# Optimization experiments

Measured on AMD Instinct MI355X. Metric: run time of the kernel, lower is better.

## Reference

```python
import jax, jax.numpy as jnp
import numpy as np

V = 30000      # vocab_size
D = 300        # t_embed
H = 4          # GATv2 heads
C = 300        # per-head out channels (hidden_dim = t_embed)
HID = 768      # hidden_size
B = 2
T = 800
NEG = 0.2      # GATv2 negative_slope default


def gatv2_layer(x, src, dst, Wl, bl, Wr, br, att, bias):
    """PyG GATv2Conv, eval mode, add_self_loops=True, concat=True.
    x: [N, Fin]; src/dst: [E] (src->dst message flow).
    Wl/Wr: [Fin, H*C]; bl/br: [H*C]; att: [H, C]; bias: [H*C].
    """
    N = x.shape[0]
    xl = (x @ Wl + bl).reshape(N, H, C)   # source transform
    xr = (x @ Wr + br).reshape(N, H, C)   # target transform
    loops = jnp.arange(N)
    s = jnp.concatenate([src, loops])
    d = jnp.concatenate([dst, loops])
    e = jax.nn.leaky_relu(xl[s] + xr[d], NEG)          # [E', H, C]
    logits = jnp.einsum('ehc,hc->eh', e, att)           # [E', H]
    # scatter-softmax over incoming edges per target node
    mx = jax.ops.segment_max(logits, d, num_segments=N)  # [N, H]
    ex = jnp.exp(logits - mx[d])
    den = jax.ops.segment_sum(ex, d, num_segments=N)
    alpha = ex / den[d]                                   # [E', H]
    out = jax.ops.segment_sum(alpha[:, :, None] * xl[s], d, num_segments=N)
    return out.reshape(N, H * C) + bias


def setup_inputs() -> dict:
    key = jax.random.key(0)
    ks = jax.random.split(key, 20)
    sc = 0.05
    inp = {
        'kg_enc_input': jax.random.randint(ks[0], (B, T, 3), 0, V),
        'embeddings': jax.random.normal(ks[1], (V, D), jnp.float32),
        # conv1: GATv2Conv(D, C, heads=H)
        'Wl1': jax.random.normal(ks[2], (D, H * C), jnp.float32) * sc,
        'bl1': jnp.zeros((H * C,), jnp.float32),
        'Wr1': jax.random.normal(ks[3], (D, H * C), jnp.float32) * sc,
        'br1': jnp.zeros((H * C,), jnp.float32),
        'att1': jax.random.normal(ks[4], (H, C), jnp.float32) * sc,
        'bias1': jnp.zeros((H * C,), jnp.float32),
        # conv2: GATv2Conv(4*C, C, heads=H)
        'Wl2': jax.random.normal(ks[5], (H * C, H * C), jnp.float32) * sc,
        'bl2': jnp.zeros((H * C,), jnp.float32),
        'Wr2': jax.random.normal(ks[6], (H * C, H * C), jnp.float32) * sc,
        'br2': jnp.zeros((H * C,), jnp.float32),
        'att2': jax.random.normal(ks[7], (H, C), jnp.float32) * sc,
        'bias2': jnp.zeros((H * C,), jnp.float32),
        # post_mp: Linear(4*C, C) -> Dropout -> Linear(C, D)
        'Wp1': jax.random.normal(ks[8], (H * C, C), jnp.float32) * sc,
        'bp1': jnp.zeros((C,), jnp.float32),
        'Wp2': jax.random.normal(ks[9], (C, D), jnp.float32) * sc,
        'bp2': jnp.zeros((D,), jnp.float32),
        # lii: Linear(3*D, HID, bias=False)
        'Wlii': jax.random.normal(ks[10], (3 * D, HID), jnp.float32) * sc,
    }
    return inp


def reference(kg_enc_input, embeddings, Wl1, bl1, Wr1, br1, att1, bias1,
              Wl2, bl2, Wr2, br2, att2, bias2, Wp1, bp1, Wp2, bp2, Wlii):
    # original GAT.forward detaches x -> no grad to embedding table
    x0 = jax.lax.stop_gradient(embeddings)

    def per_sample(kg):  # kg: [T, 3]
        head, rel, tail = kg[:, 0], kg[:, 1], kg[:, 2]
        # edge_list = cat([[head;rel], [rel;tail]], dim=1)
        src = jnp.concatenate([head, rel])
        dst = jnp.concatenate([rel, tail])
        h = gatv2_layer(x0, src, dst, Wl1, bl1, Wr1, br1, att1, bias1)
        h = jax.nn.relu(h)                 # dropout: eval mode, identity
        h = gatv2_layer(h, src, dst, Wl2, bl2, Wr2, br2, att2, bias2)
        h = jax.nn.relu(h)
        w = (h @ Wp1 + bp1) @ Wp2 + bp2    # post_mp, [V, D]
        # per-triple gather + concat of (h, r, t) node embeddings
        return jnp.concatenate([w[head], w[rel], w[tail]], axis=-1)  # [T, 3D]

    final = jax.vmap(per_sample)(kg_enc_input)   # [B, T, 3D]
    return final @ Wlii                           # [B, T, HID]
```

## Files before the change

kernel.cpp:

```cpp
#include <hip/hip_runtime.h>
#include <hip/hip_bf16.h>

#define V 30000
#define D 300
#define H 4
#define C 300
#define HC 1200
#define B 2
#define T 800
#define E 1600
#define MAXM 2400
#define NEG 0.2f
#define SCAN_CH ((MAXM + 255) / 256)

#define MR 2432
#define KD 320
#define KHC 1216
#define NLR 2432
#define WB_LD 320
#define KF2 960

typedef __attribute__((ext_vector_type(8))) unsigned short u16x8;
typedef __attribute__((ext_vector_type(8))) short s16x8;
typedef __attribute__((ext_vector_type(4))) float f32x4;

__device__ inline unsigned short f2b(float v) {
    unsigned u = __float_as_uint(v);
    unsigned r = (u + 0x7FFFu + ((u >> 16) & 1u)) >> 16;
    return (unsigned short)r;
}
__device__ inline float b2f(unsigned short u) {
    return __uint_as_float(((unsigned)u) << 16);
}

#define GLOAD_LDS16(g, l) __builtin_amdgcn_global_load_lds( \
    (const __attribute__((address_space(1))) void*)(g), \
    (__attribute__((address_space(3))) void*)(l), 16, 0, 0)


__global__ void k_init(int* map, int* list, int* mcnt) {
    int i = blockIdx.x * blockDim.x + threadIdx.x;
    if (i < B * V) map[i] = -1;
    if (i < B * MAXM) list[i] = 0;
    if (i < B) mcnt[i] = 0;
}

__global__ void k_mark(const int* __restrict__ kg, int* map) {
    int i = blockIdx.x * blockDim.x + threadIdx.x;
    if (i >= B * T * 3) return;
    int b = i / (T * 3);
    map[b * V + kg[i]] = 1;
}

__global__ void k_compact(int* map, int* list, int* mcnt) {
    int b = blockIdx.y;
    int i = blockIdx.x * 256 + threadIdx.x;
    bool pred = (i < V) && (map[b * V + i] == 1);
    unsigned long long m = __ballot(pred);
    int lane = threadIdx.x & 63;
    int wid = threadIdx.x >> 6;
    __shared__ int wcnt[4];
    __shared__ int base;
    if (lane == 0) wcnt[wid] = __popcll(m);
    __syncthreads();
    if (threadIdx.x == 0) {
        int t = 0;
#pragma unroll
        for (int w2 = 0; w2 < 4; ++w2) { int c = wcnt[w2]; wcnt[w2] = t; t += c; }
        base = t ? atomicAdd(&mcnt[b], t) : 0;
    }
    __syncthreads();
    if (pred) {
        int idx = base + wcnt[wid] + __popcll(m & ((1ull << lane) - 1ull));
        map[b * V + i] = idx;
        list[b * MAXM + idx] = i;
    }
}

__global__ __launch_bounds__(256) void k_graph(const int* __restrict__ kg,
                                               const int* __restrict__ map,
                                               int* __restrict__ off_g,
                                               int* __restrict__ csr,
                                               int* __restrict__ tric) {
    int b = blockIdx.x;
    int tid = threadIdx.x;
    __shared__ int sdeg[MAXM];
    __shared__ int soff[MAXM + 1];
    __shared__ int ses[E];
    __shared__ int sed[E];
    __shared__ int ts[256];
    for (int j = tid; j < MAXM; j += 256) sdeg[j] = 0;
    __syncthreads();
    for (int t = tid; t < T; t += 256) {
        const int* kk = kg + ((long)b * T + t) * 3;
        int hc = map[b * V + kk[0]];
        int rc = map[b * V + kk[1]];
        int tc = map[b * V + kk[2]];
        ses[t] = hc;     sed[t] = rc;
        ses[T + t] = rc; sed[T + t] = tc;
        atomicAdd(&sdeg[rc], 1);
        atomicAdd(&sdeg[tc], 1);
        int* tr = tric + ((long)b * T + t) * 3;
        tr[0] = hc; tr[1] = rc; tr[2] = tc;
    }
    __syncthreads();
    int base = tid * SCAN_CH;
    int loc[SCAN_CH];
    int sum = 0;
#pragma unroll
    for (int j = 0; j < SCAN_CH; ++j) {
        int v = (base + j < MAXM) ? sdeg[base + j] : 0;
        sum += v; loc[j] = sum;
    }
    ts[tid] = sum; __syncthreads();
    for (int s = 1; s < 256; s <<= 1) {
        int v = (tid >= s) ? ts[tid - s] : 0;
        __syncthreads();
        ts[tid] += v;
        __syncthreads();
    }
    int excl = (tid > 0) ? ts[tid - 1] : 0;
#pragma unroll
    for (int j = 0; j < SCAN_CH; ++j)
        if (base + j < MAXM) soff[base + j + 1] = excl + loc[j];
    if (tid == 0) soff[0] = 0;
    __syncthreads();
    for (int j = tid; j < MAXM; j += 256) sdeg[j] = 0;
    __syncthreads();
    for (int e = tid; e < E; e += 256) {
        int d = sed[e];
        int pos = soff[d] + atomicAdd(&sdeg[d], 1);
        csr[b * E + pos] = ses[e];
    }
    for (int j = tid; j <= MAXM; j += 256) off_g[b * (MAXM + 1) + j] = soff[j];
}

__global__ void k_wt_all(const float* __restrict__ Wl1, const float* __restrict__ Wr1,
                         const float* __restrict__ Wl2, const float* __restrict__ Wr2,
                         const float* __restrict__ Wp1, const float* __restrict__ Wp2,
                         const float* __restrict__ Wlii,
                         const float* __restrict__ bl1, const float* __restrict__ br1,
                         const float* __restrict__ bl2, const float* __restrict__ br2,
                         const float* __restrict__ bp1, const float* __restrict__ bp2,
                         unsigned short* Wlr1t, unsigned short* Wlr2t,
                         unsigned short* Wp2t, unsigned short* Wp1b,
                         unsigned short* Wft2,
                         float* blr1, float* blr2, float* bp12) {
    const int KT[6]  = {10, 10, 38, 38, 10, 30};
    const int CUM[10] = {0, 380, 760, 2204, 3648, 3748, 4468, 4508, 4518, 4520};
    int bid = blockIdx.x;
    int task = 0;
    while (bid >= CUM[task + 1]) ++task;
    int local = bid - CUM[task];
    int tx = threadIdx.x, ty = threadIdx.y;
    int tid = ty * 32 + tx;

    if (task == 6) {
        int r0 = local * 32;
#pragma unroll
        for (int p = 0; p < 4; ++p) {
            int row = r0 + ty + p * 8;
#pragma unroll
            for (int j = 0; j < 10; ++j) {
                int c = tx + j * 32;
                unsigned short v = 0;
                if (row < 1200 && c < 300) v = f2b(Wp1[(long)row * 300 + c]);
                Wp1b[(long)row * 320 + c] = v;
            }
        }
        return;
    }
    if (task == 7) {
        int c = local * 256 + tid;
        if (c < NLR) {
            float v1 = 0.f, v2 = 0.f;
            if (c < 1200) { v1 = bl1[c]; v2 = bl2[c]; }
            else if (c >= 1216 && c < 2416) { v1 = br1[c - 1216]; v2 = br2[c - 1216]; }
            blr1[c] = v1; blr2[c] = v2;
        }
        return;
    }
    if (task == 8) {
        int n = local * 256 + tid;
        if (n < 300) {
            float s = bp2[n];
            for (int m = 0; m < 300; ++m) s += bp1[m] * Wp2[(long)m * 300 + n];
            bp12[n] = s;
        }
        return;
    }

    __shared__ float t[32][33];
    if (task == 5) {
        int kt = local % 30, nt = local / 30;
        int k0 = kt * 32, n0 = nt * 32;
#pragma unroll
        for (int p = 0; p < 4; ++p) {
            int gk = k0 + ty + p * 8, n = n0 + tx;
            int pp = (gk >= 640) ? 2 : (gk >= 320 ? 1 : 0);
            int kc = gk - pp * 320;
            t[ty + p * 8][tx] = (kc < 300) ? Wlii[(long)(300 * pp + kc) * 768 + n] : 0.f;
        }
        __syncthreads();
#pragma unroll
        for (int p = 0; p < 4; ++p) {
            int n = n0 + ty + p * 8, gk = k0 + tx;
            Wft2[(long)n * 960 + gk] = f2b(t[tx][ty + p * 8]);
        }
        return;
    }

    int kt = local % KT[task], nt = local / KT[task];
    const float* W; unsigned short* Wt; int K, N, Kp;
    switch (task) {
        case 0: W = Wl1;  Wt = Wlr1t;                     K = 300;  N = 1200; Kp = KD;  break;
        case 1: W = Wr1;  Wt = Wlr1t + (long)1216 * KD;   K = 300;  N = 1200; Kp = KD;  break;
        case 2: W = Wl2;  Wt = Wlr2t;                     K = 1200; N = 1200; Kp = KHC; break;
        case 3: W = Wr2;  Wt = Wlr2t + (long)1216 * KHC;  K = 1200; N = 1200; Kp = KHC; break;
        default: W = Wp2; Wt = Wp2t;                      K = 300;  N = 300;  Kp = KD;  break;
    }
    int k0 = kt * 32, n0 = nt * 32;
#pragma unroll
    for (int p = 0; p < 4; ++p) {
        int k = k0 + ty + p * 8, n = n0 + tx;
        t[ty + p * 8][tx] = (k < K && n < N) ? W[(long)k * N + n] : 0.f;
    }
    __syncthreads();
#pragma unroll
    for (int p = 0; p < 4; ++p) {
        int n = n0 + ty + p * 8, k = k0 + tx;
        Wt[(long)n * Kp + k] = f2b(t[tx][ty + p * 8]);
    }
}

__global__ void k_embgather(const float* __restrict__ emb, const int* __restrict__ list,
                            unsigned short* __restrict__ Eb) {
    int b = blockIdx.y, i = blockIdx.x;
    int src = list[b * MAXM + i];
    const float* e = emb + (long)src * D;
    unsigned short* o = Eb + ((long)b * MR + i) * KD;
    int c = threadIdx.x;
    if (c < 75) {
        float4 v = *(const float4*)(e + c * 4);
        ushort4 u;
        u.x = f2b(v.x); u.y = f2b(v.y); u.z = f2b(v.z); u.w = f2b(v.w);
        *(ushort4*)(o + c * 4) = u;
    } else if (c < 80) {
        *(ushort4*)(o + c * 4) = make_ushort4(0, 0, 0, 0);
    }
}

__device__ inline void tile_decode(int& m0, int& n0) {
    int nbx = gridDim.x, nby = gridDim.y;
    int nwg = nbx * nby;
    int wg = blockIdx.y * nbx + blockIdx.x;
    int q = nwg >> 3, r8 = nwg & 7;
    int xcd = wg & 7, idx = wg >> 3;
    int L = (xcd < r8 ? xcd * (q + 1) : r8 * (q + 1) + (xcd - r8) * q) + idx;
    const int G = 4;
    int band = L / (G * nbx);
    int first = band * G;
    int sz = min(G, nby - first);
    int rem = L - band * G * nbx;
    int by = first + rem % sz;
    int bx = rem / sz;
    m0 = by * 128; n0 = bx * 128;
}

__global__ __launch_bounds__(256) void k_mgemm(
    const unsigned short* __restrict__ A, long sA, int lda,
    const unsigned short* __restrict__ Wt, int ldw,
    const float* __restrict__ bias,
    int M, int N, int K,
    float* __restrict__ outF, long sF, int ldf,
    unsigned short* __restrict__ outB, long sB, int ldb_) {
    int b = blockIdx.z;
    A += (long)b * sA;
    __shared__ unsigned short As[2][128][32];
    __shared__ unsigned short Bs[2][128][32];
    int tid = threadIdx.x;
    int m0, n0; tile_decode(m0, n0);

    int w = tid >> 6, lane = tid & 63;
    int wr = (w >> 1) * 64, wc = (w & 1) * 64;
    int fr = lane & 15, fq = lane >> 4;
    int r0 = tid >> 2, sg = tid & 3;
    int swz = (sg ^ ((r0 >> 1) & 3)) * 8;
    const unsigned short* Ap  = A  + (long)(m0 + r0) * lda + swz;
    const unsigned short* Ap2 = A  + (long)(m0 + r0 + 64) * lda + swz;
    const unsigned short* Bp  = Wt + (long)(n0 + r0) * ldw + swz;
    const unsigned short* Bp2 = Wt + (long)(n0 + r0 + 64) * ldw + swz;

    f32x4 acc[4][4] = {};
    GLOAD_LDS16(Ap,  &As[0][r0][sg * 8]);
    GLOAD_LDS16(Ap2, &As[0][r0 + 64][sg * 8]);
    GLOAD_LDS16(Bp,  &Bs[0][r0][sg * 8]);
    GLOAD_LDS16(Bp2, &Bs[0][r0 + 64][sg * 8]);
    __syncthreads();
    int cur = 0;
    for (int k0 = 0; k0 < K; k0 += 32) {
        int nxt = cur ^ 1;
        if (k0 + 32 < K) {
            GLOAD_LDS16(Ap + k0 + 32,  &As[nxt][r0][sg * 8]);
            GLOAD_LDS16(Ap2 + k0 + 32, &As[nxt][r0 + 64][sg * 8]);
            GLOAD_LDS16(Bp + k0 + 32,  &Bs[nxt][r0][sg * 8]);
            GLOAD_LDS16(Bp2 + k0 + 32, &Bs[nxt][r0 + 64][sg * 8]);
        }
        s16x8 af[4], bfr[4];
#pragma unroll
        for (int m = 0; m < 4; ++m) {
            int rr = wr + m * 16 + fr;
            af[m] = *(const s16x8*)&As[cur][rr][(fq ^ ((rr >> 1) & 3)) * 8];
        }
#pragma unroll
        for (int n = 0; n < 4; ++n) {
            int rr = wc + n * 16 + fr;
            bfr[n] = *(const s16x8*)&Bs[cur][rr][(fq ^ ((rr >> 1) & 3)) * 8];
        }
#pragma unroll
        for (int m = 0; m < 4; ++m)
#pragma unroll
            for (int n = 0; n < 4; ++n)
                acc[m][n] = __builtin_amdgcn_mfma_f32_16x16x32_bf16(af[m], bfr[n], acc[m][n], 0, 0, 0);
        __syncthreads();
        cur = nxt;
    }
    float* oF = outF ? outF + (long)b * sF : nullptr;
    unsigned short* oB = outB ? outB + (long)b * sB : nullptr;
#pragma unroll
    for (int m = 0; m < 4; ++m) {
        int rb = m0 + wr + m * 16 + fq * 4;
#pragma unroll
        for (int n = 0; n < 4; ++n) {
            int col = n0 + wc + n * 16 + fr;
#pragma unroll
            for (int j = 0; j < 4; ++j) {
                int row = rb + j;
                if (row >= M) continue;
                if (col < N) {
                    float v = acc[m][n][j] + (bias ? bias[col] : 0.f);
                    if (oF) oF[(long)row * ldf + col] = v;
                    if (oB) oB[(long)row * ldb_ + col] = f2b(v);
                } else if (oB && col < ldb_) {
                    oB[(long)row * ldb_ + col] = 0;
                }
            }
        }
    }
}

__global__ __launch_bounds__(256) void k_fgemm(
    const unsigned short* __restrict__ wb, long sW,
    const int* __restrict__ tric,
    const unsigned short* __restrict__ Wft2,
    float* __restrict__ out) {
    int b = blockIdx.z;
    const unsigned short* wB = wb + (long)b * sW;
    const int* tr = tric + (long)b * T * 3;
    float* oF = out + (long)b * T * 768;
    __shared__ unsigned short As[2][128][32];
    __shared__ unsigned short Bs[2][128][32];
    int tid = threadIdx.x;
    int m0, n0; tile_decode(m0, n0);

    int w = tid >> 6, lane = tid & 63;
    int wr = (w >> 1) * 64, wc = (w & 1) * 64;
    int fr = lane & 15, fq = lane >> 4;
    int r0 = tid >> 2, sg = tid & 3;
    int swz = (sg ^ ((r0 >> 1) & 3)) * 8;

    int gm  = m0 + r0;
    int gm2 = gm + 64;
    int t1 = min(gm, T - 1) * 3, t2 = min(gm2, T - 1) * 3;
    int tr_a[3] = {tr[t1], tr[t1 + 1], tr[t1 + 2]};
    int tr_b[3] = {tr[t2], tr[t2 + 1], tr[t2 + 2]};

    const unsigned short* Bp  = Wft2 + (long)(n0 + r0) * KF2 + swz;
    const unsigned short* Bp2 = Wft2 + (long)(n0 + r0 + 64) * KF2 + swz;

    auto stage = [&](int buf, int k0) {
        int kk = k0 + swz;
        int p_ = (kk >= 640) ? 2 : (kk >= 320 ? 1 : 0);
        int kc = kk - p_ * 320;
        GLOAD_LDS16(wB + (long)tr_a[p_] * WB_LD + kc, &As[buf][r0][sg * 8]);
        GLOAD_LDS16(wB + (long)tr_b[p_] * WB_LD + kc, &As[buf][r0 + 64][sg * 8]);
        GLOAD_LDS16(Bp + k0,  &Bs[buf][r0][sg * 8]);
        GLOAD_LDS16(Bp2 + k0, &Bs[buf][r0 + 64][sg * 8]);
    };

    f32x4 acc[4][4] = {};
    stage(0, 0);
    __syncthreads();
    int cur = 0;
    for (int k0 = 0; k0 < KF2; k0 += 32) {
        int nxt = cur ^ 1;
        if (k0 + 32 < KF2) stage(nxt, k0 + 32);
        s16x8 af[4], bfr[4];
#pragma unroll
        for (int m = 0; m < 4; ++m) {
            int rr = wr + m * 16 + fr;
            af[m] = *(const s16x8*)&As[cur][rr][(fq ^ ((rr >> 1) & 3)) * 8];
        }
#pragma unroll
        for (int n = 0; n < 4; ++n) {
            int rr = wc + n * 16 + fr;
            bfr[n] = *(const s16x8*)&Bs[cur][rr][(fq ^ ((rr >> 1) & 3)) * 8];
        }
#pragma unroll
        for (int m = 0; m < 4; ++m)
#pragma unroll
            for (int n = 0; n < 4; ++n)
                acc[m][n] = __builtin_amdgcn_mfma_f32_16x16x32_bf16(af[m], bfr[n], acc[m][n], 0, 0, 0);
        __syncthreads();
        cur = nxt;
    }
#pragma unroll
    for (int m = 0; m < 4; ++m) {
        int rb = m0 + wr + m * 16 + fq * 4;
#pragma unroll
        for (int n = 0; n < 4; ++n) {
            int col = n0 + wc + n * 16 + fr;
#pragma unroll
            for (int j = 0; j < 4; ++j) {
                int row = rb + j;
                if (row < T) oF[(long)row * 768 + col] = acc[m][n][j];
            }
        }
    }
}

__global__ __launch_bounds__(256) void k_att(
    const unsigned short* __restrict__ XLR,
    const int* __restrict__ off, const int* __restrict__ csr,
    const float* __restrict__ att, const float* __restrict__ bias,
    unsigned short* __restrict__ OUT) {
    const long sX = (long)MR * NLR;
    const long sO = (long)MR * KHC;
    int b = blockIdx.y;
    int i = blockIdx.x;
    const unsigned short* xl = XLR + (long)b * sX;
    const unsigned short* xr = xl + 1216;
    unsigned short* out = OUT + (long)b * sO;
    int lane = threadIdx.x & 63;
    int h = threadIdx.x >> 6;
    int c0 = lane * 4;
    int c1 = 256 + c0;
    bool tail = lane < 11;

    float xrf[8], attf[8];
    {
        const unsigned short* xp = xr + (long)i * NLR + h * C;
        ushort4 u0 = *(const ushort4*)(xp + c0);
        ushort4 u1 = tail ? *(const ushort4*)(xp + c1) : make_ushort4(0, 0, 0, 0);
        xrf[0] = b2f(u0.x); xrf[1] = b2f(u0.y); xrf[2] = b2f(u0.z); xrf[3] = b2f(u0.w);
        xrf[4] = b2f(u1.x); xrf[5] = b2f(u1.y); xrf[6] = b2f(u1.z); xrf[7] = b2f(u1.w);
        float4 a0 = *(const float4*)(att + h * C + c0);
        attf[0] = a0.x; attf[1] = a0.y; attf[2] = a0.z; attf[3] = a0.w;
        if (tail) {
            float4 a1 = *(const float4*)(att + h * C + c1);
            attf[4] = a1.x; attf[5] = a1.y; attf[6] = a1.z; attf[7] = a1.w;
        } else { attf[4] = attf[5] = attf[6] = attf[7] = 0.f; }
    }
    int o0 = off[b * (MAXM + 1) + i];
    int dg = off[b * (MAXM + 1) + i + 1] - o0;
    const int* cs = csr + b * E;

    float mx = -3e38f, den = 0.f;
    float acc[8] = {0.f, 0.f, 0.f, 0.f, 0.f, 0.f, 0.f, 0.f};
    auto step = [&](int s) {
        const unsigned short* xp = xl + (long)s * NLR + h * C;
        ushort4 v0 = *(const ushort4*)(xp + c0);
        ushort4 v1 = tail ? *(const ushort4*)(xp + c1) : make_ushort4(0, 0, 0, 0);
        float xv[8];
        xv[0] = b2f(v0.x); xv[1] = b2f(v0.y); xv[2] = b2f(v0.z); xv[3] = b2f(v0.w);
        xv[4] = b2f(v1.x); xv[5] = b2f(v1.y); xv[6] = b2f(v1.z); xv[7] = b2f(v1.w);
        float part = 0.f;
#pragma unroll
        for (int j = 0; j < 8; ++j) {
            float v = xv[j] + xrf[j];
            v = v > 0.f ? v : NEG * v;
            part += attf[j] * v;
        }
#pragma unroll
        for (int m = 1; m < 64; m <<= 1) part += __shfl_xor(part, m);
        float mn = fmaxf(mx, part);
        float sc = __expf(mx - mn);
        float p = __expf(part - mn);
        den = den * sc + p;
#pragma unroll
        for (int j = 0; j < 8; ++j) acc[j] = acc[j] * sc + p * xv[j];
        mx = mn;
    };
    step(i);
    for (int e = 0; e < dg; ++e) step(cs[o0 + e]);

    float inv = 1.f / den;
    unsigned short* op = out + (long)i * KHC + h * C;
    {
        float4 b0 = *(const float4*)(bias + h * C + c0);
        ushort4 s0;
        float v;
        v = acc[0] * inv + b0.x; s0.x = f2b(v > 0.f ? v : 0.f);
        v = acc[1] * inv + b0.y; s0.y = f2b(v > 0.f ? v : 0.f);
        v = acc[2] * inv + b0.z; s0.z = f2b(v > 0.f ? v : 0.f);
        v = acc[3] * inv + b0.w; s0.w = f2b(v > 0.f ? v : 0.f);
        *(ushort4*)(op + c0) = s0;
        if (tail) {
            float4 b1 = *(const float4*)(bias + h * C + c1);
            ushort4 s1;
            v = acc[4] * inv + b1.x; s1.x = f2b(v > 0.f ? v : 0.f);
            v = acc[5] * inv + b1.y; s1.y = f2b(v > 0.f ? v : 0.f);
            v = acc[6] * inv + b1.z; s1.z = f2b(v > 0.f ? v : 0.f);
            v = acc[7] * inv + b1.w; s1.w = f2b(v > 0.f ? v : 0.f);
            *(ushort4*)(op + c1) = s1;
        }
    }
    if (h == 0 && lane < KHC - HC)
        out[(long)i * KHC + HC + lane] = 0;
}

extern "C" void kernel_launch(void* const* d_in, const int* in_sizes, int n_in,
                              void* d_out, int out_size, void* d_ws, size_t ws_size,
                              hipStream_t stream) {
    const int*   kg    = (const int*)d_in[0];
    const float* emb   = (const float*)d_in[1];
    const float* Wl1   = (const float*)d_in[2];
    const float* bl1   = (const float*)d_in[3];
    const float* Wr1   = (const float*)d_in[4];
    const float* br1   = (const float*)d_in[5];
    const float* att1  = (const float*)d_in[6];
    const float* bias1 = (const float*)d_in[7];
    const float* Wl2   = (const float*)d_in[8];
    const float* bl2   = (const float*)d_in[9];
    const float* Wr2   = (const float*)d_in[10];
    const float* br2   = (const float*)d_in[11];
    const float* att2  = (const float*)d_in[12];
    const float* bias2 = (const float*)d_in[13];
    const float* Wp1   = (const float*)d_in[14];
    const float* bp1   = (const float*)d_in[15];
    const float* Wp2   = (const float*)d_in[16];
    const float* bp2   = (const float*)d_in[17];
    const float* Wlii  = (const float*)d_in[18];
    float* out = (float*)d_out;

    char* ws = (char*)d_ws;
    size_t o = 0;
    auto alloc = [&](size_t bytes) -> void* {
        void* p = ws + o;
        o = (o + bytes + 255) & ~(size_t)255;
        return p;
    };
    int* map  = (int*)alloc(sizeof(int) * B * V);
    int* list = (int*)alloc(sizeof(int) * B * MAXM);
    int* mcnt = (int*)alloc(sizeof(int) * B);
    int* off  = (int*)alloc(sizeof(int) * B * (MAXM + 1));
    int* csr  = (int*)alloc(sizeof(int) * B * E);
    int* tric = (int*)alloc(sizeof(int) * B * T * 3);

    long sXlr = (long)MR * NLR;
    long sHb  = (long)MR * KHC;
    long sEb  = (long)MR * KD;
    unsigned short* Xlr = (unsigned short*)alloc(2LL * B * sXlr);
    unsigned short* Hb  = (unsigned short*)alloc(2LL * B * sHb);
    unsigned short* Eb  = (unsigned short*)alloc(2LL * B * sEb);

    unsigned short* Wlr1t = (unsigned short*)alloc(2LL * 2432 * KD);
    unsigned short* Wlr2t = (unsigned short*)alloc(2LL * 2432 * KHC);
    unsigned short* Wp2t  = (unsigned short*)alloc(2LL * 384 * KD);
    unsigned short* Wp1b  = (unsigned short*)alloc(2LL * 1280 * 320);
    unsigned short* Wp12t = (unsigned short*)alloc(2LL * 384 * KHC);
    unsigned short* Wft2  = (unsigned short*)alloc(2LL * 768 * KF2);
    float* blr1 = (float*)alloc(sizeof(float) * NLR);
    float* blr2 = (float*)alloc(sizeof(float) * NLR);
    float* bp12 = (float*)alloc(sizeof(float) * 384);
    (void)ws_size; (void)in_sizes; (void)n_in; (void)out_size;

    unsigned short* wb = Eb;

    k_init<<<(B * V + 255) / 256, 256, 0, stream>>>(map, list, mcnt);
    k_mark<<<(B * T * 3 + 255) / 256, 256, 0, stream>>>(kg, map);
    k_compact<<<dim3((V + 255) / 256, B), 256, 0, stream>>>(map, list, mcnt);
    k_graph<<<B, 256, 0, stream>>>(kg, map, off, csr, tric);

    k_wt_all<<<4520, dim3(32, 8), 0, stream>>>(Wl1, Wr1, Wl2, Wr2, Wp1, Wp2, Wlii,
                                               bl1, br1, bl2, br2, bp1, bp2,
                                               Wlr1t, Wlr2t, Wp2t, Wp1b, Wft2,
                                               blr1, blr2, bp12);

    k_embgather<<<dim3(MAXM, B), 128, 0, stream>>>(emb, list, Eb);

    k_mgemm<<<dim3(10, 3, 1), 256, 0, stream>>>(Wp2t, 0, KD, Wp1b, 320, nullptr,
                                                300, 1216, KD,
                                                nullptr, 0, 0, Wp12t, 0, KHC);

    long sWb = (long)MR * WB_LD;

    dim3 gL(19, 19, B);
    k_mgemm<<<gL, 256, 0, stream>>>(Eb, sEb, KD, Wlr1t, KD, blr1, MAXM, NLR, KD,
                                    nullptr, 0, 0, Xlr, sXlr, NLR);
    k_att<<<dim3(MAXM, B), 256, 0, stream>>>(Xlr, off, csr, att1, bias1, Hb);
    k_mgemm<<<gL, 256, 0, stream>>>(Hb, sHb, KHC, Wlr2t, KHC, blr2, MAXM, NLR, KHC,
                                    nullptr, 0, 0, Xlr, sXlr, NLR);
    k_att<<<dim3(MAXM, B), 256, 0, stream>>>(Xlr, off, csr, att2, bias2, Hb);
    k_mgemm<<<dim3(3, 19, B), 256, 0, stream>>>(Hb, sHb, KHC, Wp12t, KHC, bp12,
                                                MAXM, 300, KHC,
                                                nullptr, 0, 0, wb, sWb, WB_LD);
    k_fgemm<<<dim3(6, 7, B), 256, 0, stream>>>(wb, sWb, tric, Wft2, out);
}
```

Baseline: 328.5 us.

## Triple-buffer GEMM k-loop with one barrier and stage output tile through LDS

Both MFMA GEMM kernels move from double to triple buffering. Loads are issued two stages ahead, and each k-step does one explicit vmcnt wait plus a single barrier instead of two __syncthreads, so more global latency is hidden. The generic GEMM now writes its bf16 output tile into LDS and then stores it as coalesced 16-byte vectors. The init kernel is replaced by hipMemsetAsync calls. The cost is more LDS per block (48KB versus 32KB), which may reduce occupancy, and the row guard is dropped, relying on padded buffers.

```diff
diff --git a/kernel.cpp b/kernel.cpp
--- a/kernel.cpp
+++ b/kernel.cpp
@@ -37,13 +37,6 @@
     (const __attribute__((address_space(1))) void*)(g), \
     (__attribute__((address_space(3))) void*)(l), 16, 0, 0)
 
-
-__global__ void k_init(int* map, int* list, int* mcnt) {
-    int i = blockIdx.x * blockDim.x + threadIdx.x;
-    if (i < B * V) map[i] = -1;
-    if (i < B * MAXM) list[i] = 0;
-    if (i < B) mcnt[i] = 0;
-}
 
 __global__ void k_mark(const int* __restrict__ kg, int* map) {
     int i = blockIdx.x * blockDim.x + threadIdx.x;
@@ -271,13 +264,11 @@
     const unsigned short* __restrict__ A, long sA, int lda,
     const unsigned short* __restrict__ Wt, int ldw,
     const float* __restrict__ bias,
-    int M, int N, int K,
-    float* __restrict__ outF, long sF, int ldf,
+    int N, int K,
     unsigned short* __restrict__ outB, long sB, int ldb_) {
     int b = blockIdx.z;
     A += (long)b * sA;
-    __shared__ unsigned short As[2][128][32];
-    __shared__ unsigned short Bs[2][128][32];
+    __shared__ unsigned short lds[3 * 8192];
     int tid = threadIdx.x;
     int m0, n0; tile_decode(m0, n0);
 
@@ -291,61 +282,72 @@
     const unsigned short* Bp  = Wt + (long)(n0 + r0) * ldw + swz;
     const unsigned short* Bp2 = Wt + (long)(n0 + r0 + 64) * ldw + swz;
 
+    auto stage = [&](int buf, int k0) {
+        unsigned short* a_ = lds + buf * 4096;
+        unsigned short* b_ = lds + 12288 + buf * 4096;
+        GLOAD_LDS16(Ap + k0,  a_ + r0 * 32 + sg * 8);
+        GLOAD_LDS16(Ap2 + k0, a_ + (r0 + 64) * 32 + sg * 8);
+        GLOAD_LDS16(Bp + k0,  b_ + r0 * 32 + sg * 8);
+        GLOAD_LDS16(Bp2 + k0, b_ + (r0 + 64) * 32 + sg * 8);
+    };
+
     f32x4 acc[4][4] = {};
-    GLOAD_LDS16(Ap,  &As[0][r0][sg * 8]);
-    GLOAD_LDS16(Ap2, &As[0][r0 + 64][sg * 8]);
-    GLOAD_LDS16(Bp,  &Bs[0][r0][sg * 8]);
-    GLOAD_LDS16(Bp2, &Bs[0][r0 + 64][sg * 8]);
-    __syncthreads();
-    int cur = 0;
-    for (int k0 = 0; k0 < K; k0 += 32) {
-        int nxt = cur ^ 1;
-        if (k0 + 32 < K) {
-            GLOAD_LDS16(Ap + k0 + 32,  &As[nxt][r0][sg * 8]);
-            GLOAD_LDS16(Ap2 + k0 + 32, &As[nxt][r0 + 64][sg * 8]);
-            GLOAD_LDS16(Bp + k0 + 32,  &Bs[nxt][r0][sg * 8]);
-            GLOAD_LDS16(Bp2 + k0 + 32, &Bs[nxt][r0 + 64][sg * 8]);
-        }
+    int NT = K >> 5;
+    stage(0, 0);
+    stage(1, 32);
+    int cur = 0, stg = 2;
+    for (int i = 0; i < NT; ++i) {
+        if (i + 1 < NT) asm volatile("s_waitcnt vmcnt(4)" ::: "memory");
+        else            asm volatile("s_waitcnt vmcnt(0)" ::: "memory");
+        __builtin_amdgcn_s_barrier();
+        __builtin_amdgcn_sched_barrier(0);
+        if (i + 2 < NT) stage(stg, (i + 2) << 5);
+        const unsigned short* a_ = lds + cur * 4096;
+        const unsigned short* b_ = lds + 12288 + cur * 4096;
         s16x8 af[4], bfr[4];
 #pragma unroll
         for (int m = 0; m < 4; ++m) {
             int rr = wr + m * 16 + fr;
-            af[m] = *(const s16x8*)&As[cur][rr][(fq ^ ((rr >> 1) & 3)) * 8];
+            af[m] = *(const s16x8*)&a_[rr * 32 + (fq ^ ((rr >> 1) & 3)) * 8];
         }
 #pragma unroll
         for (int n = 0; n < 4; ++n) {
             int rr = wc + n * 16 + fr;
-            bfr[n] = *(const s16x8*)&Bs[cur][rr][(fq ^ ((rr >> 1) & 3)) * 8];
+            bfr[n] = *(const s16x8*)&b_[rr * 32 + (fq ^ ((rr >> 1) & 3)) * 8];
         }
 #pragma unroll
         for (int m = 0; m < 4; ++m)
 #pragma unroll
             for (int n = 0; n < 4; ++n)
                 acc[m][n] = __builtin_amdgcn_mfma_f32_16x16x32_bf16(af[m], bfr[n], acc[m][n], 0, 0, 0);
-        __syncthreads();
-        cur = nxt;
-    }
-    float* oF = outF ? outF + (long)b * sF : nullptr;
-    unsigned short* oB = outB ? outB + (long)b * sB : nullptr;
+        cur = (cur == 2) ? 0 : cur + 1;
+        stg = (stg == 2) ? 0 : stg + 1;
+    }
+    __syncthreads();
 #pragma unroll
     for (int m = 0; m < 4; ++m) {
-        int rb = m0 + wr + m * 16 + fq * 4;
+        int rl = wr + m * 16 + fq * 4;
 #pragma unroll
         for (int n = 0; n < 4; ++n) {
-            int col = n0 + wc + n * 16 + fr;
+            int cl = wc + n * 16 + fr;
+            int colg = n0 + cl;
+            float bi = (colg < N && bias) ? bias[colg] : 0.f;
 #pragma unroll
             for (int j = 0; j < 4; ++j) {
-                int row = rb + j;
-                if (row >= M) continue;
-                if (col < N) {
-                    float v = acc[m][n][j] + (bias ? bias[col] : 0.f);
-                    if (oF) oF[(long)row * ldf + col] = v;
-                    if (oB) oB[(long)row * ldb_ + col] = f2b(v);
-                } else if (oB && col < ldb_) {
-                    oB[(long)row * ldb_ + col] = 0;
-                }
+                unsigned short v = (colg < N) ? f2b(acc[m][n][j] + bi) : (unsigned short)0;
+                lds[(rl + j) * 128 + cl] = v;
             }
         }
+    }
+    __syncthreads();
+    unsigned short* oB = outB + (long)b * sB;
+#pragma unroll
+    for (int q = 0; q < 8; ++q) {
+        int idx = q * 256 + tid;
+        int row = idx >> 4, c8 = idx & 15;
+        int colg = n0 + c8 * 8;
+        if (colg < ldb_)
+            *(u16x8*)(oB + (long)(m0 + row) * ldb_ + colg) = *(const u16x8*)&lds[row * 128 + c8 * 8];
     }
 }
 
@@ -358,8 +360,7 @@
     const unsigned short* wB = wb + (long)b * sW;
     const int* tr = tric + (long)b * T * 3;
     float* oF = out + (long)b * T * 768;
-    __shared__ unsigned short As[2][128][32];
-    __shared__ unsigned short Bs[2][128][32];
+    __shared__ unsigned short lds[3 * 8192];
     int tid = threadIdx.x;
     int m0, n0; tile_decode(m0, n0);
 
@@ -379,40 +380,48 @@
     const unsigned short* Bp2 = Wft2 + (long)(n0 + r0 + 64) * KF2 + swz;
 
     auto stage = [&](int buf, int k0) {
+        unsigned short* a_ = lds + buf * 4096;
+        unsigned short* b_ = lds + 12288 + buf * 4096;
         int kk = k0 + swz;
         int p_ = (kk >= 640) ? 2 : (kk >= 320 ? 1 : 0);
         int kc = kk - p_ * 320;
-        GLOAD_LDS16(wB + (long)tr_a[p_] * WB_LD + kc, &As[buf][r0][sg * 8]);
-        GLOAD_LDS16(wB + (long)tr_b[p_] * WB_LD + kc, &As[buf][r0 + 64][sg * 8]);
-        GLOAD_LDS16(Bp + k0,  &Bs[buf][r0][sg * 8]);
-        GLOAD_LDS16(Bp2 + k0, &Bs[buf][r0 + 64][sg * 8]);
+        GLOAD_LDS16(wB + (long)tr_a[p_] * WB_LD + kc, a_ + r0 * 32 + sg * 8);
+        GLOAD_LDS16(wB + (long)tr_b[p_] * WB_LD + kc, a_ + (r0 + 64) * 32 + sg * 8);
+        GLOAD_LDS16(Bp + k0,  b_ + r0 * 32 + sg * 8);
+        GLOAD_LDS16(Bp2 + k0, b_ + (r0 + 64) * 32 + sg * 8);
     };
 
     f32x4 acc[4][4] = {};
+    const int NT = KF2 >> 5;
     stage(0, 0);
-    __syncthreads();
-    int cur = 0;
-    for (int k0 = 0; k0 < KF2; k0 += 32) {
-        int nxt = cur ^ 1;
-        if (k0 + 32 < KF2) stage(nxt, k0 + 32);
+    stage(1, 32);
+    int cur = 0, stg = 2;
+    for (int i = 0; i < NT; ++i) {
+        if (i + 1 < NT) asm volatile("s_waitcnt vmcnt(4)" ::: "memory");
+        else            asm volatile("s_waitcnt vmcnt(0)" ::: "memory");
+        __builtin_amdgcn_s_barrier();
+        __builtin_amdgcn_sched_barrier(0);
+        if (i + 2 < NT) stage(stg, (i + 2) << 5);
+        const unsigned short* a_ = lds + cur * 4096;
+        const unsigned short* b_ = lds + 12288 + cur * 4096;
         s16x8 af[4], bfr[4];
 #pragma unroll
         for (int m = 0; m < 4; ++m) {
             int rr = wr + m * 16 + fr;
-            af[m] = *(const s16x8*)&As[cur][rr][(fq ^ ((rr >> 1) & 3)) * 8];
+            af[m] = *(const s16x8*)&a_[rr * 32 + (fq ^ ((rr >> 1) & 3)) * 8];
         }
 #pragma unroll
         for (int n = 0; n < 4; ++n) {
             int rr = wc + n * 16 + fr;
-            bfr[n] = *(const s16x8*)&Bs[cur][rr][(fq ^ ((rr >> 1) & 3)) * 8];
+            bfr[n] = *(const s16x8*)&b_[rr * 32 + (fq ^ ((rr >> 1) & 3)) * 8];
         }
 #pragma unroll
         for (int m = 0; m < 4; ++m)
 #pragma unroll
             for (int n = 0; n < 4; ++n)
                 acc[m][n] = __builtin_amdgcn_mfma_f32_16x16x32_bf16(af[m], bfr[n], acc[m][n], 0, 0, 0);
-        __syncthreads();
-        cur = nxt;
+        cur = (cur == 2) ? 0 : cur + 1;
+        stg = (stg == 2) ? 0 : stg + 1;
     }
 #pragma unroll
     for (int m = 0; m < 4; ++m) {
@@ -577,7 +586,9 @@
 
     unsigned short* wb = Eb;
 
-    k_init<<<(B * V + 255) / 256, 256, 0, stream>>>(map, list, mcnt);
+    hipMemsetAsync(map, 0xFF, sizeof(int) * B * V, stream);
+    hipMemsetAsync(list, 0, sizeof(int) * B * MAXM, stream);
+    hipMemsetAsync(mcnt, 0, sizeof(int) * B, stream);
     k_mark<<<(B * T * 3 + 255) / 256, 256, 0, stream>>>(kg, map);
     k_compact<<<dim3((V + 255) / 256, B), 256, 0, stream>>>(map, list, mcnt);
     k_graph<<<B, 256, 0, stream>>>(kg, map, off, csr, tric);
@@ -590,20 +601,18 @@
     k_embgather<<<dim3(MAXM, B), 128, 0, stream>>>(emb, list, Eb);
 
     k_mgemm<<<dim3(10, 3, 1), 256, 0, stream>>>(Wp2t, 0, KD, Wp1b, 320, nullptr,
-                                                300, 1216, KD,
-                                                nullptr, 0, 0, Wp12t, 0, KHC);
+                                                1216, KD, Wp12t, 0, KHC);
 
     long sWb = (long)MR * WB_LD;
 
     dim3 gL(19, 19, B);
-    k_mgemm<<<gL, 256, 0, stream>>>(Eb, sEb, KD, Wlr1t, KD, blr1, MAXM, NLR, KD,
-                                    nullptr, 0, 0, Xlr, sXlr, NLR);
+    k_mgemm<<<gL, 256, 0, stream>>>(Eb, sEb, KD, Wlr1t, KD, blr1,
+                                    NLR, KD, Xlr, sXlr, NLR);
     k_att<<<dim3(MAXM, B), 256, 0, stream>>>(Xlr, off, csr, att1, bias1, Hb);
-    k_mgemm<<<gL, 256, 0, stream>>>(Hb, sHb, KHC, Wlr2t, KHC, blr2, MAXM, NLR, KHC,
-                                    nullptr, 0, 0, Xlr, sXlr, NLR);
+    k_mgemm<<<gL, 256, 0, stream>>>(Hb, sHb, KHC, Wlr2t, KHC, blr2,
+                                    NLR, KHC, Xlr, sXlr, NLR);
     k_att<<<dim3(MAXM, B), 256, 0, stream>>>(Xlr, off, csr, att2, bias2, Hb);
     k_mgemm<<<dim3(3, 19, B), 256, 0, stream>>>(Hb, sHb, KHC, Wp12t, KHC, bp12,
-                                                MAXM, 300, KHC,
-                                                nullptr, 0, 0, wb, sWb, WB_LD);
+                                                300, KHC, wb, sWb, WB_LD);
     k_fgemm<<<dim3(6, 7, B), 256, 0, stream>>>(wb, sWb, tric, Wft2, out);
 }
```

Measured after the change: 284.0 us. -13.6%, faster.
